# Kernel optimization log

Hardware: AMD Instinct MI355X
Metric: run time of the kernel (lower is better)

The kernel has to match this reference:

```python
import jax, jax.numpy as jnp
import numpy as np

IN_C, OUT_C, K, STRIDE, PAD = 128, 256, 3, 1, 1

def setup_inputs() -> dict:
    key = jax.random.key(0)
    kx, kw = jax.random.split(key)
    X = jax.random.normal(kx, (32, IN_C, 56, 56), dtype=jnp.float32)
    # kaiming_uniform_ default: bound = sqrt(6 / fan_in), fan_in = in_c * K * K
    fan_in = IN_C * K * K
    bound = float(np.sqrt(6.0 / fan_in))
    kernel = jax.random.uniform(kw, (OUT_C, IN_C, K, K), dtype=jnp.float32,
                                minval=-bound, maxval=bound)
    return {"X": X, "kernel": kernel}

def reference(X, kernel) -> jnp.ndarray:
    # Cross-correlation conv2d, NCHW / OIHW, stride=STRIDE, symmetric zero pad.
    return jax.lax.conv_general_dilated(
        X, kernel,
        window_strides=(STRIDE, STRIDE),
        padding=((PAD, PAD), (PAD, PAD)),
        dimension_numbers=("NCHW", "OIHW", "NCHW"),
    )
```

## Files before the change

### kernel.cpp

```cpp
#include <hip/hip_runtime.h>
#include <hip/hip_bf16.h>


#define IC 128
#define OC 256
#define HH 56
#define WW 56
#define NB 32
#define PH 58
#define PW 58
#define PS (PH*PW)
#define NPIX (HH*WW)
#define GPIX (NB*NPIX)
#define KDIM (IC*9)

#define BMH 128
#define BNP 448

#define WROWB 3712
#define WINREAL 37120
#define WINB 37888

typedef short  bf16x8 __attribute__((ext_vector_type(8)));
typedef float  f32x4  __attribute__((ext_vector_type(4)));
typedef unsigned int u32;

__device__ __forceinline__ unsigned short f2bf(float f) {
  union { float f; unsigned int u; } c; c.f = f;
  unsigned int u = c.u;
  u += 0x7FFFu + ((u >> 16) & 1u);
  return (unsigned short)(u >> 16);
}

__device__ __forceinline__ void gload16(const unsigned short* g, unsigned short* l) {
  __builtin_amdgcn_global_load_lds(
      (const __attribute__((address_space(1))) u32*)g,
      (__attribute__((address_space(3))) u32*)l, 16, 0, 0);
}

__device__ __forceinline__ int swz(int a) { return a ^ (((a >> 8) & 15) << 4); }

__global__ __launch_bounds__(256) void zero_border(unsigned short* __restrict__ Xt, int total) {
  int idx = blockIdx.x * 256 + threadIdx.x;
  if (idx >= total) return;
  int e  = idx & 127;
  int b  = idx >> 7;
  int n  = b / 228;
  int bp = b - n * 228;
  int y, x;
  if (bp < 58)       { y = 0;  x = bp; }
  else if (bp < 116) { y = 57; x = bp - 58; }
  else {
    int b2 = bp - 116;
    y = 1 + (b2 >> 1);
    x = (b2 & 1) * 57;
  }
  Xt[((long)(n * PH + y) * PW + x) * IC + e] = 0;
}

__global__ __launch_bounds__(256) void pad_x_nhwc(const float* __restrict__ X,
                                                  unsigned short* __restrict__ Xt) {
  __shared__ float tile[128][65];
  const int t   = threadIdx.x;
  const int p0  = blockIdx.x * 64;
  const int n   = p0 / NPIX;
  const int rem = p0 - n * NPIX;

  const int pixl = t & 63;
  const int q    = t >> 6;
  const float* src = X + ((long)n * IC + q) * NPIX + rem + pixl;
  #pragma unroll
  for (int i = 0; i < 32; ++i)
    tile[q + i * 4][pixl] = src[(long)i * 4 * NPIX];
  __syncthreads();

  const int pix = t >> 2;
  const int icq = (t & 3) * 32;
  int p = rem + pix;
  int y = p / WW, x = p - y * WW;
  unsigned short* dst = Xt + ((long)(n * PH + y + 1) * PW + (x + 1)) * IC + icq;
  #pragma unroll
  for (int g = 0; g < 4; ++g) {
    bf16x8 v;
    #pragma unroll
    for (int j = 0; j < 8; ++j)
      ((unsigned short*)&v)[j] = f2bf(tile[icq + g * 8 + j][pix]);
    *reinterpret_cast<bf16x8*>(dst + g * 8) = v;
  }
}

__global__ __launch_bounds__(256) void pack_w(const float* __restrict__ W,
                                              unsigned short* __restrict__ Wb, int total) {
  int idx = blockIdx.x * 256 + threadIdx.x;
  if (idx >= total) return;
  int e  = idx & 7;
  int oc = (idx >> 3) & 255;
  int s  = (idx >> 11) & 15;
  int t  = idx >> 15;
  Wb[idx] = f2bf(W[(oc * IC + s * 8 + e) * 9 + t]);
}

__global__ __launch_bounds__(512) void conv_win(
    const unsigned short* __restrict__ Xt,
    const unsigned short* __restrict__ Wb,
    float* __restrict__ out) {
  __shared__ __align__(16) unsigned short lds[37888];
  char* const ldsb = (char*)lds;

  const int tid  = threadIdx.x;
  const int lane = tid & 63;
  const int w    = tid >> 6;
  const int wm = w >> 2, wn = w & 3;
  const int l15 = lane & 15, lh = lane >> 4;

  const int bid   = blockIdx.x;
  const int wg    = (bid & 7) * 56 + (bid >> 3);
  const int ntile = wg >> 1;
  const int mhalf = wg & 1;
  const int n   = ntile / 7;
  const int rg  = ntile - n * 7;
  const int y0  = rg * 8;
  const int ocb = mhalf * BMH;

  const unsigned short* aBase = Wb + (size_t)lh * 2048 + (ocb + wm * 64 + l15) * 8;

  const unsigned short* srcW[5];
  #pragma unroll
  for (int r = 0; r < 5; ++r) {
    int xw = swz((tid + r * 512) * 16);
    if (xw >= WINREAL) xw = WINREAL - 16;
    int row = xw / WROWB;
    int rem = xw - row * WROWB;
    int col = rem >> 6;
    srcW[r] = Xt + ((long)((n * PH + y0 + row) * PW + col)) * IC + ((rem & 63) >> 1);
  }

  int pixLin[7];
  #pragma unroll
  for (int j = 0; j < 7; ++j) {
    int local = wn * 112 + j * 16 + l15;
    int wy = local / 56, wx = local - wy * 56;
    pixLin[j] = (wy * 58 + wx) * 64 + lh * 16;
  }

  f32x4 acc[4][7];
  #pragma unroll
  for (int m = 0; m < 4; ++m)
    #pragma unroll
    for (int j = 0; j < 7; ++j)
      acc[m][j] = (f32x4){0.f, 0.f, 0.f, 0.f};

  auto stageWin = [&](int icb) {
    char* base = ldsb + (icb & 1) * WINB + (tid & ~63) * 16;
    #pragma unroll
    for (int r = 0; r < 5; ++r)
      if (r < 4 || w <= 4)
        gload16(srcW[r] + icb * 32, (unsigned short*)(base + r * 8192));
  };

  stageWin(0);
  bf16x8 aReg[2][4];
  #pragma unroll
  for (int m = 0; m < 4; ++m)
    aReg[0][m] = *(const bf16x8*)(aBase + m * 128);
  asm volatile("s_waitcnt vmcnt(0)" ::: "memory");
  __builtin_amdgcn_s_barrier();
  __builtin_amdgcn_sched_barrier(0);

  for (int icb = 0; icb < 4; ++icb) {
    const int winSel = (icb & 1) * WINB;

    #pragma unroll
    for (int tap = 0; tap < 9; ++tap) {
      const int rs = (icb + tap) & 1;
      const int ps = rs ^ 1;

      if (tap < 8) {
        #pragma unroll
        for (int m = 0; m < 4; ++m)
          aReg[ps][m] = *(const bf16x8*)(aBase + (size_t)(tap + 1) * 32768
                                               + (size_t)icb * 8192 + m * 128);
      } else if (icb < 3) {
        #pragma unroll
        for (int m = 0; m < 4; ++m)
          aReg[ps][m] = *(const bf16x8*)(aBase + (size_t)(icb + 1) * 8192 + m * 128);
      }

      const int dy = tap / 3, dx = tap - dy * 3;
      const int toff = (dy * 58 + dx) * 64;

      bf16x8 bfv[7];
      #pragma unroll
      for (int j = 0; j < 7; ++j)
        bfv[j] = *(const bf16x8*)(ldsb + winSel + swz(pixLin[j] + toff));

      __builtin_amdgcn_s_setprio(1);
      #pragma unroll
      for (int j = 0; j < 7; ++j)
        #pragma unroll
        for (int m = 0; m < 4; ++m)
          acc[m][j] = __builtin_amdgcn_mfma_f32_16x16x32_bf16(aReg[rs][m], bfv[j],
                                                              acc[m][j], 0, 0, 0);
      __builtin_amdgcn_s_setprio(0);

      if (tap == 4 && icb < 3) stageWin(icb + 1);
    }

    asm volatile("s_waitcnt vmcnt(0)" ::: "memory");
    __builtin_amdgcn_s_barrier();
    __builtin_amdgcn_sched_barrier(0);
  }

  #pragma unroll
  for (int j = 0; j < 7; ++j) {
    int local = wn * 112 + j * 16 + l15;
    int pidx  = rg * BNP + local;
    #pragma unroll
    for (int m = 0; m < 4; ++m) {
      int oc = ocb + wm * 64 + m * 16 + lh * 4;
      float* op = out + ((long)(n * OC + oc)) * NPIX + pidx;
      #pragma unroll
      for (int r = 0; r < 4; ++r)
        op[(long)r * NPIX] = acc[m][j][r];
    }
  }
}

__global__ __launch_bounds__(256) void conv_naive(const float* __restrict__ X,
                                                  const float* __restrict__ W,
                                                  float* __restrict__ out, int total) {
  int idx = blockIdx.x * 256 + threadIdx.x;
  if (idx >= total) return;
  int prow = idx % NPIX;
  int t    = idx / NPIX;
  int oc   = t % OC;
  int n    = t / OC;
  int oh = prow / WW, ow = prow % WW;
  float s = 0.f;
  for (int ic = 0; ic < IC; ++ic) {
    const float* xp = X + ((long)(n * IC + ic)) * NPIX;
    const float* wp = W + ((long)(oc * IC + ic)) * 9;
    #pragma unroll
    for (int kh = 0; kh < 3; ++kh) {
      int ih = oh + kh - 1;
      if (ih < 0 || ih >= HH) continue;
      #pragma unroll
      for (int kw = 0; kw < 3; ++kw) {
        int iw = ow + kw - 1;
        if (iw < 0 || iw >= WW) continue;
        s += xp[ih * WW + iw] * wp[kh * 3 + kw];
      }
    }
  }
  out[idx] = s;
}

extern "C" void kernel_launch(void* const* d_in, const int* in_sizes, int n_in,
                              void* d_out, int out_size, void* d_ws, size_t ws_size,
                              hipStream_t stream) {
  const float* X = (const float*)d_in[0];
  const float* W = (const float*)d_in[1];
  float* out = (float*)d_out;

  const size_t xt_elems = (size_t)NB * PS * IC;
  const size_t wb_elems = (size_t)9 * 16 * 256 * 8;
  const size_t need = (xt_elems + wb_elems) * sizeof(unsigned short);

  if (ws_size >= need) {
    unsigned short* Xt = (unsigned short*)d_ws;
    unsigned short* Wb = Xt + xt_elems;

    int totB = NB * 228 * IC;
    zero_border<<<(totB + 255) / 256, 256, 0, stream>>>(Xt, totB);
    pad_x_nhwc<<<GPIX / 64, 256, 0, stream>>>(X, Xt);
    int totW = (int)wb_elems;
    pack_w<<<(totW + 255) / 256, 256, 0, stream>>>(W, Wb, totW);
    conv_win<<<(GPIX / BNP) * (OC / BMH), 512, 0, stream>>>(Xt, Wb, out);
  } else {
    int tot = NB * OC * NPIX;
    conv_naive<<<(tot + 255) / 256, 256, 0, stream>>>(X, W, out, tot);
  }
}
```

Baseline: 85.24 us.

## Retile conv to 256 output channels by 64 pixels per block for occupancy

The conv kernel's block tile changes from 128 output channels by 448 pixels (8 rows) to all 256 output channels by a 64-pixel window. This shrinks the LDS input window and the per-wave accumulators (4x2 instead of 4x7), and adds launch bounds asking for 4 blocks per SM, so that more waves fit per CU and the grid grows to 1568 blocks. In exchange, each block reuses weights over fewer pixels, so weight traffic from global memory/L2 rises sharply, and each input halo is reloaded more often relative to its size. The window prefetch is also moved later, to tap 7.

```diff
diff --git a/kernel.cpp b/kernel.cpp
--- a/kernel.cpp
+++ b/kernel.cpp
@@ -14,12 +14,10 @@
 #define GPIX (NB*NPIX)
 #define KDIM (IC*9)
 
-#define BMH 128
-#define BNP 448
-
+#define BNP 64
 #define WROWB 3712
-#define WINREAL 37120
-#define WINB 37888
+#define WINREAL 14848
+#define WINB 16384
 
 typedef short  bf16x8 __attribute__((ext_vector_type(8)));
 typedef float  f32x4  __attribute__((ext_vector_type(4)));
@@ -100,62 +98,59 @@
   Wb[idx] = f2bf(W[(oc * IC + s * 8 + e) * 9 + t]);
 }
 
-__global__ __launch_bounds__(512) void conv_win(
+__global__ __launch_bounds__(512, 4) void conv_win(
     const unsigned short* __restrict__ Xt,
     const unsigned short* __restrict__ Wb,
     float* __restrict__ out) {
-  __shared__ __align__(16) unsigned short lds[37888];
+  __shared__ __align__(16) unsigned short lds[16384];
   char* const ldsb = (char*)lds;
 
   const int tid  = threadIdx.x;
   const int lane = tid & 63;
   const int w    = tid >> 6;
-  const int wm = w >> 2, wn = w & 3;
+  const int wm = w >> 1, wn = w & 1;
   const int l15 = lane & 15, lh = lane >> 4;
 
-  const int bid   = blockIdx.x;
-  const int wg    = (bid & 7) * 56 + (bid >> 3);
-  const int ntile = wg >> 1;
-  const int mhalf = wg & 1;
-  const int n   = ntile / 7;
-  const int rg  = ntile - n * 7;
-  const int y0  = rg * 8;
-  const int ocb = mhalf * BMH;
-
-  const unsigned short* aBase = Wb + (size_t)lh * 2048 + (ocb + wm * 64 + l15) * 8;
-
-  const unsigned short* srcW[5];
-  #pragma unroll
-  for (int r = 0; r < 5; ++r) {
+  const int bid = blockIdx.x;
+  const int wg  = (bid & 7) * 196 + (bid >> 3);
+  const int n   = wg / 49;
+  const int p0  = (wg - n * 49) * BNP;
+  const int r0  = p0 / 56;
+
+  const unsigned short* aBase = Wb + (size_t)lh * 2048 + (wm * 64 + l15) * 8;
+
+  const unsigned short* srcW[2];
+  #pragma unroll
+  for (int r = 0; r < 2; ++r) {
     int xw = swz((tid + r * 512) * 16);
     if (xw >= WINREAL) xw = WINREAL - 16;
     int row = xw / WROWB;
     int rem = xw - row * WROWB;
     int col = rem >> 6;
-    srcW[r] = Xt + ((long)((n * PH + y0 + row) * PW + col)) * IC + ((rem & 63) >> 1);
-  }
-
-  int pixLin[7];
-  #pragma unroll
-  for (int j = 0; j < 7; ++j) {
-    int local = wn * 112 + j * 16 + l15;
-    int wy = local / 56, wx = local - wy * 56;
+    srcW[r] = Xt + ((long)((n * PH + r0 + row) * PW + col)) * IC + ((rem & 63) >> 1);
+  }
+
+  int pixLin[2];
+  #pragma unroll
+  for (int j = 0; j < 2; ++j) {
+    int local = wn * 32 + j * 16 + l15;
+    int p  = p0 + local;
+    int wy = p / 56 - r0;
+    int wx = p - (p / 56) * 56;
     pixLin[j] = (wy * 58 + wx) * 64 + lh * 16;
   }
 
-  f32x4 acc[4][7];
+  f32x4 acc[4][2];
   #pragma unroll
   for (int m = 0; m < 4; ++m)
     #pragma unroll
-    for (int j = 0; j < 7; ++j)
+    for (int j = 0; j < 2; ++j)
       acc[m][j] = (f32x4){0.f, 0.f, 0.f, 0.f};
 
   auto stageWin = [&](int icb) {
     char* base = ldsb + (icb & 1) * WINB + (tid & ~63) * 16;
-    #pragma unroll
-    for (int r = 0; r < 5; ++r)
-      if (r < 4 || w <= 4)
-        gload16(srcW[r] + icb * 32, (unsigned short*)(base + r * 8192));
+    gload16(srcW[0] + icb * 32, (unsigned short*)(base));
+    gload16(srcW[1] + icb * 32, (unsigned short*)(base + 8192));
   };
 
   stageWin(0);
@@ -189,21 +184,21 @@
       const int dy = tap / 3, dx = tap - dy * 3;
       const int toff = (dy * 58 + dx) * 64;
 
-      bf16x8 bfv[7];
-      #pragma unroll
-      for (int j = 0; j < 7; ++j)
+      bf16x8 bfv[2];
+      #pragma unroll
+      for (int j = 0; j < 2; ++j)
         bfv[j] = *(const bf16x8*)(ldsb + winSel + swz(pixLin[j] + toff));
 
       __builtin_amdgcn_s_setprio(1);
       #pragma unroll
-      for (int j = 0; j < 7; ++j)
+      for (int j = 0; j < 2; ++j)
         #pragma unroll
         for (int m = 0; m < 4; ++m)
           acc[m][j] = __builtin_amdgcn_mfma_f32_16x16x32_bf16(aReg[rs][m], bfv[j],
                                                               acc[m][j], 0, 0, 0);
       __builtin_amdgcn_s_setprio(0);
 
-      if (tap == 4 && icb < 3) stageWin(icb + 1);
+      if (tap == 7 && icb < 3) stageWin(icb + 1);
     }
 
     asm volatile("s_waitcnt vmcnt(0)" ::: "memory");
@@ -212,12 +207,11 @@
   }
 
   #pragma unroll
-  for (int j = 0; j < 7; ++j) {
-    int local = wn * 112 + j * 16 + l15;
-    int pidx  = rg * BNP + local;
+  for (int j = 0; j < 2; ++j) {
+    int pidx = p0 + wn * 32 + j * 16 + l15;
     #pragma unroll
     for (int m = 0; m < 4; ++m) {
-      int oc = ocb + wm * 64 + m * 16 + lh * 4;
+      int oc = wm * 64 + m * 16 + lh * 4;
       float* op = out + ((long)(n * OC + oc)) * NPIX + pidx;
       #pragma unroll
       for (int r = 0; r < 4; ++r)
@@ -275,7 +269,7 @@
     pad_x_nhwc<<<GPIX / 64, 256, 0, stream>>>(X, Xt);
     int totW = (int)wb_elems;
     pack_w<<<(totW + 255) / 256, 256, 0, stream>>>(W, Wb, totW);
-    conv_win<<<(GPIX / BNP) * (OC / BMH), 512, 0, stream>>>(Xt, Wb, out);
+    conv_win<<<GPIX / BNP, 512, 0, stream>>>(Xt, Wb, out);
   } else {
     int tot = NB * OC * NPIX;
     conv_naive<<<(tot + 255) / 256, 256, 0, stream>>>(X, W, out, tot);
```

After: 106.4 us. 24.8% more time.

## Shrink conv blocks to 64 output channels and use planar LDS window layout

Applied to the files above, without the earlier changes.

Each block now covers 64 output channels with 4 waves (256 threads) instead of 128 channels with 8 waves, which doubles the grid and the number of times each input window is staged. The LDS window moves from a swizzled pixel-major layout to four 8-channel planes with a padded plane stride, removing the XOR swizzle arithmetic. The LDS B-fragment reads are issued before the weight register prefetch. The aim is better occupancy and cheaper addressing, at the cost of twice the global input traffic and possible LDS bank conflicts from the unswizzled planes.

```diff
diff --git a/kernel.cpp b/kernel.cpp
--- a/kernel.cpp
+++ b/kernel.cpp
@@ -14,11 +14,8 @@
 #define GPIX (NB*NPIX)
 #define KDIM (IC*9)
 
-#define BMH 128
 #define BNP 448
-
-#define WROWB 3712
-#define WINREAL 37120
+#define PLSTR 9312
 #define WINB 37888
 
 typedef short  bf16x8 __attribute__((ext_vector_type(8)));
@@ -37,8 +34,6 @@
       (const __attribute__((address_space(1))) u32*)g,
       (__attribute__((address_space(3))) u32*)l, 16, 0, 0);
 }
-
-__device__ __forceinline__ int swz(int a) { return a ^ (((a >> 8) & 15) << 4); }
 
 __global__ __launch_bounds__(256) void zero_border(unsigned short* __restrict__ Xt, int total) {
   int idx = blockIdx.x * 256 + threadIdx.x;
@@ -100,7 +95,7 @@
   Wb[idx] = f2bf(W[(oc * IC + s * 8 + e) * 9 + t]);
 }
 
-__global__ __launch_bounds__(512) void conv_win(
+__global__ __launch_bounds__(256) void conv_win(
     const unsigned short* __restrict__ Xt,
     const unsigned short* __restrict__ Wb,
     float* __restrict__ out) {
@@ -110,29 +105,29 @@
   const int tid  = threadIdx.x;
   const int lane = tid & 63;
   const int w    = tid >> 6;
-  const int wm = w >> 2, wn = w & 3;
+  const int wn   = w;
   const int l15 = lane & 15, lh = lane >> 4;
 
-  const int bid   = blockIdx.x;
-  const int wg    = (bid & 7) * 56 + (bid >> 3);
-  const int ntile = wg >> 1;
-  const int mhalf = wg & 1;
-  const int n   = ntile / 7;
-  const int rg  = ntile - n * 7;
+  const int bid = blockIdx.x;
+  const int wg  = (bid & 7) * 112 + (bid >> 3);
+  const int pt  = wg >> 2;
+  const int ocb = (wg & 3) * 64;
+  const int n   = pt / 7;
+  const int rg  = pt - n * 7;
   const int y0  = rg * 8;
-  const int ocb = mhalf * BMH;
-
-  const unsigned short* aBase = Wb + (size_t)lh * 2048 + (ocb + wm * 64 + l15) * 8;
-
-  const unsigned short* srcW[5];
-  #pragma unroll
-  for (int r = 0; r < 5; ++r) {
-    int xw = swz((tid + r * 512) * 16);
-    if (xw >= WINREAL) xw = WINREAL - 16;
-    int row = xw / WROWB;
-    int rem = xw - row * WROWB;
-    int col = rem >> 6;
-    srcW[r] = Xt + ((long)((n * PH + y0 + row) * PW + col)) * IC + ((rem & 63) >> 1);
+
+  const unsigned short* aBase = Wb + (size_t)lh * 2048 + (ocb + l15) * 8;
+
+  const unsigned short* srcW[10];
+  #pragma unroll
+  for (int r = 0; r < 10; ++r) {
+    int slot = (r < 9) ? (r * 256 + tid) : (2304 + lane);
+    int x = slot * 16;
+    int plane = x / PLSTR; if (plane > 3) plane = 3;
+    int rem = x - plane * PLSTR; if (rem >= 9280) rem = 9264;
+    int pix = rem >> 4;
+    int row = pix / 58, col = pix - row * 58;
+    srcW[r] = Xt + ((long)((n * PH + y0 + row) * PW + col)) * IC + plane * 8;
   }
 
   int pixLin[7];
@@ -140,7 +135,7 @@
   for (int j = 0; j < 7; ++j) {
     int local = wn * 112 + j * 16 + l15;
     int wy = local / 56, wx = local - wy * 56;
-    pixLin[j] = (wy * 58 + wx) * 64 + lh * 16;
+    pixLin[j] = lh * PLSTR + (wy * 58 + wx) * 16;
   }
 
   f32x4 acc[4][7];
@@ -153,9 +148,9 @@
   auto stageWin = [&](int icb) {
     char* base = ldsb + (icb & 1) * WINB + (tid & ~63) * 16;
     #pragma unroll
-    for (int r = 0; r < 5; ++r)
-      if (r < 4 || w <= 4)
-        gload16(srcW[r] + icb * 32, (unsigned short*)(base + r * 8192));
+    for (int r = 0; r < 10; ++r)
+      if (r < 9 || w == 0)
+        gload16(srcW[r] + icb * 32, (unsigned short*)(base + r * 4096));
   };
 
   stageWin(0);
@@ -174,6 +169,14 @@
     for (int tap = 0; tap < 9; ++tap) {
       const int rs = (icb + tap) & 1;
       const int ps = rs ^ 1;
+
+      const int dy = tap / 3, dx = tap - dy * 3;
+      const int toff = (dy * 58 + dx) * 16;
+
+      bf16x8 bfv[7];
+      #pragma unroll
+      for (int j = 0; j < 7; ++j)
+        bfv[j] = *(const bf16x8*)(ldsb + winSel + pixLin[j] + toff);
 
       if (tap < 8) {
         #pragma unroll
@@ -186,14 +189,6 @@
           aReg[ps][m] = *(const bf16x8*)(aBase + (size_t)(icb + 1) * 8192 + m * 128);
       }
 
-      const int dy = tap / 3, dx = tap - dy * 3;
-      const int toff = (dy * 58 + dx) * 64;
-
-      bf16x8 bfv[7];
-      #pragma unroll
-      for (int j = 0; j < 7; ++j)
-        bfv[j] = *(const bf16x8*)(ldsb + winSel + swz(pixLin[j] + toff));
-
       __builtin_amdgcn_s_setprio(1);
       #pragma unroll
       for (int j = 0; j < 7; ++j)
@@ -213,11 +208,10 @@
 
   #pragma unroll
   for (int j = 0; j < 7; ++j) {
-    int local = wn * 112 + j * 16 + l15;
-    int pidx  = rg * BNP + local;
+    int pidx = rg * BNP + wn * 112 + j * 16 + l15;
     #pragma unroll
     for (int m = 0; m < 4; ++m) {
-      int oc = ocb + wm * 64 + m * 16 + lh * 4;
+      int oc = ocb + m * 16 + lh * 4;
       float* op = out + ((long)(n * OC + oc)) * NPIX + pidx;
       #pragma unroll
       for (int r = 0; r < 4; ++r)
@@ -275,7 +269,7 @@
     pad_x_nhwc<<<GPIX / 64, 256, 0, stream>>>(X, Xt);
     int totW = (int)wb_elems;
     pack_w<<<(totW + 255) / 256, 256, 0, stream>>>(W, Wb, totW);
-    conv_win<<<(GPIX / BNP) * (OC / BMH), 512, 0, stream>>>(Xt, Wb, out);
+    conv_win<<<(GPIX / BNP) * 4, 256, 0, stream>>>(Xt, Wb, out);
   } else {
     int tot = NB * OC * NPIX;
     conv_naive<<<(tot + 255) / 256, 256, 0, stream>>>(X, W, out, tot);
```

Measured after the change: 111.6 us. 30.9% more time.

## Shrink conv tiles to 2-row, 128-thread blocks and fuse border zeroing

Applied to the files above, without the earlier changes.

Each conv_win workgroup now covers two output rows (112 pixels) by 128 output channels with two waves, down from eight rows with eight waves. The input window in LDS shrinks from about 37 KB to 16 KB, so more workgroups fit per CU and the grid grows fourfold, which should give better load balance and occupancy. The cost is more halo reloading per output, because each 2-row tile fetches 4 input rows. The separate zero_border launch is folded into pad_x_nhwc as extra blocks that write 16-byte zero vectors, removing one kernel launch.

```diff
diff --git a/kernel.cpp b/kernel.cpp
--- a/kernel.cpp
+++ b/kernel.cpp
@@ -14,12 +14,13 @@
 #define GPIX (NB*NPIX)
 #define KDIM (IC*9)
 
-#define BMH 128
-#define BNP 448
-
+#define BNP 112
 #define WROWB 3712
-#define WINREAL 37120
-#define WINB 37888
+#define WINREAL 14848
+#define WINB 16384
+
+#define PADBLK 1568
+#define BORDBLK 456
 
 typedef short  bf16x8 __attribute__((ext_vector_type(8)));
 typedef float  f32x4  __attribute__((ext_vector_type(4)));
@@ -40,26 +41,29 @@
 
 __device__ __forceinline__ int swz(int a) { return a ^ (((a >> 8) & 15) << 4); }
 
-__global__ __launch_bounds__(256) void zero_border(unsigned short* __restrict__ Xt, int total) {
-  int idx = blockIdx.x * 256 + threadIdx.x;
-  if (idx >= total) return;
-  int e  = idx & 127;
-  int b  = idx >> 7;
-  int n  = b / 228;
-  int bp = b - n * 228;
-  int y, x;
-  if (bp < 58)       { y = 0;  x = bp; }
-  else if (bp < 116) { y = 57; x = bp - 58; }
-  else {
-    int b2 = bp - 116;
-    y = 1 + (b2 >> 1);
-    x = (b2 & 1) * 57;
-  }
-  Xt[((long)(n * PH + y) * PW + x) * IC + e] = 0;
-}
-
 __global__ __launch_bounds__(256) void pad_x_nhwc(const float* __restrict__ X,
                                                   unsigned short* __restrict__ Xt) {
+  if (blockIdx.x >= PADBLK) {
+    int slot = (blockIdx.x - PADBLK) * 256 + threadIdx.x;
+    if (slot >= NB * 228 * 16) return;
+    int n  = slot / 3648;
+    int r  = slot - n * 3648;
+    int bp = r >> 4;
+    int e8 = r & 15;
+    int y, x;
+    if (bp < 58)       { y = 0;  x = bp; }
+    else if (bp < 116) { y = 57; x = bp - 58; }
+    else {
+      int b2 = bp - 116;
+      y = 1 + (b2 >> 1);
+      x = (b2 & 1) * 57;
+    }
+    bf16x8 z = (bf16x8)(short)0;
+    *reinterpret_cast<bf16x8*>(
+        Xt + ((long)(n * PH + y) * PW + x) * IC + e8 * 8) = z;
+    return;
+  }
+
   __shared__ float tile[128][65];
   const int t   = threadIdx.x;
   const int p0  = blockIdx.x * 64;
@@ -100,34 +104,32 @@
   Wb[idx] = f2bf(W[(oc * IC + s * 8 + e) * 9 + t]);
 }
 
-__global__ __launch_bounds__(512) void conv_win(
+__global__ __launch_bounds__(128) void conv_win(
     const unsigned short* __restrict__ Xt,
     const unsigned short* __restrict__ Wb,
     float* __restrict__ out) {
-  __shared__ __align__(16) unsigned short lds[37888];
+  __shared__ __align__(16) unsigned short lds[16384];
   char* const ldsb = (char*)lds;
 
   const int tid  = threadIdx.x;
   const int lane = tid & 63;
-  const int w    = tid >> 6;
-  const int wm = w >> 2, wn = w & 3;
+  const int wm   = tid >> 6;
   const int l15 = lane & 15, lh = lane >> 4;
 
-  const int bid   = blockIdx.x;
-  const int wg    = (bid & 7) * 56 + (bid >> 3);
-  const int ntile = wg >> 1;
-  const int mhalf = wg & 1;
-  const int n   = ntile / 7;
-  const int rg  = ntile - n * 7;
-  const int y0  = rg * 8;
-  const int ocb = mhalf * BMH;
+  const int bid = blockIdx.x;
+  const int wg  = (bid & 7) * 224 + (bid >> 3);
+  const int pt  = wg >> 1;
+  const int ocb = (wg & 1) * 128;
+  const int n   = pt / 28;
+  const int rt  = pt - n * 28;
+  const int y0  = rt * 2;
 
   const unsigned short* aBase = Wb + (size_t)lh * 2048 + (ocb + wm * 64 + l15) * 8;
 
-  const unsigned short* srcW[5];
-  #pragma unroll
-  for (int r = 0; r < 5; ++r) {
-    int xw = swz((tid + r * 512) * 16);
+  const unsigned short* srcW[8];
+  #pragma unroll
+  for (int r = 0; r < 8; ++r) {
+    int xw = swz((r * 128 + tid) * 16);
     if (xw >= WINREAL) xw = WINREAL - 16;
     int row = xw / WROWB;
     int rem = xw - row * WROWB;
@@ -138,7 +140,7 @@
   int pixLin[7];
   #pragma unroll
   for (int j = 0; j < 7; ++j) {
-    int local = wn * 112 + j * 16 + l15;
+    int local = j * 16 + l15;
     int wy = local / 56, wx = local - wy * 56;
     pixLin[j] = (wy * 58 + wx) * 64 + lh * 16;
   }
@@ -153,9 +155,8 @@
   auto stageWin = [&](int icb) {
     char* base = ldsb + (icb & 1) * WINB + (tid & ~63) * 16;
     #pragma unroll
-    for (int r = 0; r < 5; ++r)
-      if (r < 4 || w <= 4)
-        gload16(srcW[r] + icb * 32, (unsigned short*)(base + r * 8192));
+    for (int r = 0; r < 8; ++r)
+      gload16(srcW[r] + icb * 32, (unsigned short*)(base + r * 2048));
   };
 
   stageWin(0);
@@ -213,8 +214,7 @@
 
   #pragma unroll
   for (int j = 0; j < 7; ++j) {
-    int local = wn * 112 + j * 16 + l15;
-    int pidx  = rg * BNP + local;
+    int pidx = rt * BNP + j * 16 + l15;
     #pragma unroll
     for (int m = 0; m < 4; ++m) {
       int oc = ocb + wm * 64 + m * 16 + lh * 4;
@@ -270,12 +270,10 @@
     unsigned short* Xt = (unsigned short*)d_ws;
     unsigned short* Wb = Xt + xt_elems;
 
-    int totB = NB * 228 * IC;
-    zero_border<<<(totB + 255) / 256, 256, 0, stream>>>(Xt, totB);
-    pad_x_nhwc<<<GPIX / 64, 256, 0, stream>>>(X, Xt);
+    pad_x_nhwc<<<PADBLK + BORDBLK, 256, 0, stream>>>(X, Xt);
     int totW = (int)wb_elems;
     pack_w<<<(totW + 255) / 256, 256, 0, stream>>>(W, Wb, totW);
-    conv_win<<<(GPIX / BNP) * (OC / BMH), 512, 0, stream>>>(Xt, Wb, out);
+    conv_win<<<(GPIX / BNP) * (OC / 128), 128, 0, stream>>>(Xt, Wb, out);
   } else {
     int tot = NB * OC * NPIX;
     conv_naive<<<(tot + 255) / 256, 256, 0, stream>>>(X, W, out, tot);
```

Result: no change. 84.52 us (-0.8%).
